# Kernel tuning notes

Measured on AMD Instinct MI355X. Metric: run time of the kernel, lower is better.

## Reference

```python
import jax, jax.numpy as jnp
import numpy as np

EPS = 1e-5  # BatchNorm1d eps


def _glorot(key, shape):
    fan_in, fan_out = shape[0], shape[1]
    lim = float(np.sqrt(6.0 / (fan_in + fan_out)))
    return jax.random.uniform(key, shape, jnp.float32, -lim, lim)


def setup_inputs() -> dict:
    key = jax.random.key(0)
    ks = jax.random.split(key, 6)
    N, IN, H, OUT = 50000, 128, 64, 64
    E = 800000
    x = jax.random.normal(ks[0], (N, IN), jnp.float32)
    edge_index = jax.random.randint(ks[1], (2, E), 0, N, jnp.int64)
    return {
        "x": x,
        "edge_index": edge_index,
        "W1": _glorot(ks[2], (IN, H)),
        "b1": jnp.zeros((H,), jnp.float32),
        "gamma1": jnp.ones((H,), jnp.float32),
        "beta1": jnp.zeros((H,), jnp.float32),
        "W2": _glorot(ks[3], (H, OUT)),
        "b2": jnp.zeros((OUT,), jnp.float32),
        "gamma2": jnp.ones((OUT,), jnp.float32),
        "beta2": jnp.zeros((OUT,), jnp.float32),
    }


def _gcn_conv(x, W, b, src, dst, norm, n):
    # x' = D^{-1/2} (A + I) D^{-1/2} X W + b  (PyG GCNConv, edge_weight=None)
    h = x @ W                              # [N, F]
    msg = h[src] * norm[:, None]           # gather + scale, [E+N, F]
    out = jax.ops.segment_sum(msg, dst, num_segments=n)  # scatter-add
    return out + b


def _batch_norm(h, gamma, beta):
    # training-mode BN over node dim, biased variance (as torch uses for normalization)
    mean = h.mean(0)
    var = h.var(0)
    return (h - mean) * jax.lax.rsqrt(var + EPS) * gamma + beta


def reference(x, edge_index, W1, b1, gamma1, beta1, W2, b2, gamma2, beta2):
    n = x.shape[0]
    # add self loops
    loop = jnp.arange(n, dtype=edge_index.dtype)
    src = jnp.concatenate([edge_index[0], loop])
    dst = jnp.concatenate([edge_index[1], loop])
    # symmetric degree normalization (deg >= 1 thanks to self loops)
    deg = jax.ops.segment_sum(jnp.ones(src.shape[0], x.dtype), dst, num_segments=n)
    dinv = jax.lax.rsqrt(jnp.maximum(deg, 1e-12))
    norm = dinv[src] * dinv[dst]           # [E+N]

    # layer 1: GCNConv -> BN -> ReLU (dropout = identity in eval)
    h = _gcn_conv(x, W1, b1, src, dst, norm, n)
    h = jax.nn.relu(_batch_norm(h, gamma1, beta1))
    # layer 2: GCNConv -> BN (no activation on last layer)
    h = _gcn_conv(h, W2, b2, src, dst, norm, n)
    h = _batch_norm(h, gamma2, beta2)
    return h
```

## Files before the change

### kernel.cpp

```cpp
#include <hip/hip_runtime.h>
#include <hip/hip_fp16.h>
#include <math.h>

#define EPS 1e-5f
#define CAP 64

typedef float v4f __attribute__((ext_vector_type(4)));

__device__ __forceinline__ float xor32sum(float a) {
    return a + __shfl_xor(a, 32, 64);
}

__global__ void k_init(int* __restrict__ cnt, float* __restrict__ stats,
                       __half* __restrict__ Ylo, __half* __restrict__ Yhi,
                       unsigned short* __restrict__ csr, int N) {
    int i = blockIdx.x * blockDim.x + threadIdx.x;
    if (i < N) {
        cnt[i] = 0;
        int4* p = (int4*)(csr + (size_t)i * CAP);
#pragma unroll
        for (int k = 0; k < 8; ++k) p[k] = make_int4(-1, -1, -1, -1);
    }
    if (i < 256) stats[i] = 0.0f;
    if (i < 16) {
        ((int*)(Ylo + (size_t)N * 32))[i] = 0;
        ((int*)(Yhi + (size_t)N * 32))[i] = 0;
    }
}

__global__ __launch_bounds__(256) void k_gemm1_fill(const float* __restrict__ x,
                                                    const float* __restrict__ W1,
                                                    __half* __restrict__ Ylo,
                                                    __half* __restrict__ Yhi, int N,
                                                    const int* __restrict__ src,
                                                    const int* __restrict__ dst,
                                                    int* __restrict__ cnt,
                                                    unsigned short* __restrict__ csr,
                                                    int E, int F, int G) {
    if ((int)blockIdx.x < F) {
        int t = blockIdx.x * 256 + threadIdx.x;
        int stride = F * 256;
        for (int e = t; e < E; e += stride) {
            int d = dst[e];
            int pos = atomicAdd(&cnt[d], 1);
            if (pos < CAP)
                __builtin_nontemporal_store((unsigned short)src[e], &csr[(size_t)d * CAP + pos]);
        }
        return;
    }
    __shared__ float w[128 * 64];
    __shared__ float xs[4][8][128];
    for (int i = threadIdx.x; i < 128 * 64; i += 256) w[i] = W1[i];
    __syncthreads();
    int lane = threadIdx.x & 63;
    int wave = threadIdx.x >> 6;
    int half = lane >> 5, l = lane & 31;
    __half* Yout = half ? Yhi : Ylo;
    int gwave = (blockIdx.x - F) * 4 + wave;
    int nw = G * 4;
    for (int r0 = gwave * 8; r0 < N; r0 += nw * 8) {
        int nr = min(8, N - r0);
        for (int j = 0; j < nr; ++j)
            *(float2*)&xs[wave][j][lane * 2] =
                *(const float2*)(x + (size_t)(r0 + j) * 128 + lane * 2);
        float acc[8];
#pragma unroll
        for (int j = 0; j < 8; ++j) acc[j] = 0.f;
#pragma unroll 4
        for (int kc = 0; kc < 32; ++kc) {
            const float* wp = &w[kc * 256 + lane];
            float wk0 = wp[0], wk1 = wp[64], wk2 = wp[128], wk3 = wp[192];
#pragma unroll
            for (int j = 0; j < 8; ++j) {
                float4 xv = *(const float4*)&xs[wave][j][kc * 4];
                acc[j] += xv.x * wk0 + xv.y * wk1 + xv.z * wk2 + xv.w * wk3;
            }
        }
#pragma unroll
        for (int j = 0; j < 8; ++j)
            if (j < nr) Yout[(size_t)(r0 + j) * 32 + l] = __float2half(acc[j]);
    }
}

__global__ void k_scale(const int* __restrict__ cnt, float* __restrict__ dinv,
                        __half* __restrict__ Ylo, __half* __restrict__ Yhi, int N) {
    int i = blockIdx.x * blockDim.x + threadIdx.x;
    if (i == 0) dinv[N] = 0.0f;
    int row = i >> 2, c4 = i & 3;
    if (row >= N) return;
    float dv = rsqrtf((float)(cnt[row] + 1));
    if (c4 == 0) dinv[row] = dv;
    union U16 { uint4 u; __half2 h[4]; } t;
#pragma unroll
    for (int buf = 0; buf < 2; ++buf) {
        __half* Y = buf ? Yhi : Ylo;
        uint4* p = (uint4*)(Y + (size_t)row * 32 + c4 * 8);
        t.u = *p;
#pragma unroll
        for (int k = 0; k < 4; ++k) {
            float2 f = __half22float2(t.h[k]);
            t.h[k] = __float22half2_rn(make_float2(f.x * dv, f.y * dv));
        }
        *p = t.u;
    }
}

__global__ __launch_bounds__(256) void k_agg(const __half* __restrict__ Ylo,
                                             const __half* __restrict__ Yhi,
                                             const unsigned short* __restrict__ csr,
                                             const int* __restrict__ cnt,
                                             const float* __restrict__ dinv,
                                             float* __restrict__ H,
                                             float* __restrict__ stats, int N) {
    __shared__ float ssum[4][32], ssq[4][32];
    int half = blockIdx.x & 1;
    const __half* Y = half ? Yhi : Ylo;
    int lane = threadIdx.x & 63;
    int wave = threadIdx.x >> 6;
    int fl = lane & 3;
    int node = (lane >> 2) & 3;
    int g = lane >> 4;
    int gd = g >> 1;
    int gsh = (g & 1) << 4;
    float selfmask = (g == 0) ? 1.f : 0.f;
    int slot = (blockIdx.x >> 1) * 4 + wave;
    int nslots = (gridDim.x >> 1) * 4;
    float s[8], q[8];
#pragma unroll
    for (int j = 0; j < 8; ++j) { s[j] = 0.f; q[j] = 0.f; }
    union U16 { uint4 u; __half2 h[4]; };
    for (int base = slot * 4; base < N; base += nslots * 4) {
        int myv = base + node;
        bool vok = myv < N;
        int vs = vok ? myv : N;
        int c  = vok ? min(cnt[myv], CAP) : 0;
        float dv = dinv[vs];
        const unsigned int* crow =
            (const unsigned int*)(csr + (size_t)(vok ? myv : 0) * CAP);
        float a[8];
        {
            U16 t; t.u = *(const uint4*)(Y + (size_t)vs * 32 + fl * 8);
#pragma unroll
            for (int k = 0; k < 4; ++k) {
                float2 f = __half22float2(t.h[k]);
                a[2 * k]     = selfmask * f.x;
                a[2 * k + 1] = selfmask * f.y;
            }
        }
        for (int b = 0; b < 16; ++b) {
            if (__all(4 * b >= c)) break;
            unsigned int w = crow[2 * b + gd];
            int ent = vok ? (int)((w >> gsh) & 0xFFFFu) : 0xFFFF;
            int idx = min(ent, N);
            U16 t; t.u = *(const uint4*)(Y + (size_t)idx * 32 + fl * 8);
#pragma unroll
            for (int k = 0; k < 4; ++k) {
                float2 f = __half22float2(t.h[k]);
                a[2 * k]     += f.x;
                a[2 * k + 1] += f.y;
            }
        }
#pragma unroll
        for (int j = 0; j < 8; ++j) {
            a[j] += __shfl_xor(a[j], 16, 64);
            a[j] = xor32sum(a[j]) * dv;
        }
        if (g == 0 && vok) {
            v4f lo = {a[0], a[1], a[2], a[3]};
            v4f hi = {a[4], a[5], a[6], a[7]};
            float* dst = H + (size_t)myv * 64 + half * 32 + fl * 8;
            __builtin_nontemporal_store(lo, (v4f*)dst);
            __builtin_nontemporal_store(hi, (v4f*)(dst + 4));
        }
#pragma unroll
        for (int j = 0; j < 8; ++j) { s[j] += a[j]; q[j] += a[j] * a[j]; }
    }
#pragma unroll
    for (int j = 0; j < 8; ++j) {
        s[j] += __shfl_xor(s[j], 4, 64); s[j] += __shfl_xor(s[j], 8, 64);
        q[j] += __shfl_xor(q[j], 4, 64); q[j] += __shfl_xor(q[j], 8, 64);
    }
    if (lane < 4) {
#pragma unroll
        for (int j = 0; j < 8; ++j) {
            ssum[wave][fl * 8 + j] = s[j];
            ssq[wave][fl * 8 + j]  = q[j];
        }
    }
    __syncthreads();
    if (threadIdx.x < 32) {
        float ts = ssum[0][threadIdx.x] + ssum[1][threadIdx.x] + ssum[2][threadIdx.x] + ssum[3][threadIdx.x];
        float tq = ssq[0][threadIdx.x] + ssq[1][threadIdx.x] + ssq[2][threadIdx.x] + ssq[3][threadIdx.x];
        atomicAdd(&stats[half * 32 + threadIdx.x], ts);
        atomicAdd(&stats[64 + half * 32 + threadIdx.x], tq);
    }
}

__global__ __launch_bounds__(256) void k_gemm2(const float* __restrict__ H1,
                                               const float* __restrict__ stats,
                                               const float* __restrict__ gamma,
                                               const float* __restrict__ beta,
                                               const float* __restrict__ W2,
                                               const float* __restrict__ dinv,
                                               __half* __restrict__ Ylo,
                                               __half* __restrict__ Yhi, int N) {
    __shared__ float w[64 * 64];
    __shared__ float xs[4][64][4];
    for (int i = threadIdx.x; i < 64 * 64; i += 256) w[i] = W2[i];
    int lane = threadIdx.x & 63;
    int wave = threadIdx.x >> 6;
    int half = lane >> 5, l = lane & 31;
    __half* Yout = half ? Yhi : Ylo;
    float mean = stats[lane] / (float)N;
    float var = stats[64 + lane] / (float)N - mean * mean;
    float rstd = rsqrtf(var + EPS);
    float scale = rstd * gamma[lane];
    float shift = beta[lane] - mean * scale;
    __syncthreads();
    int gwave = blockIdx.x * 4 + wave;
    int nw = gridDim.x * 4;
    for (int r0 = gwave * 4; r0 < N; r0 += nw * 4) {
        int nr = min(4, N - r0);
#pragma unroll
        for (int j = 0; j < 4; ++j) {
            float v = 0.f;
            if (j < nr) {
                v = H1[(size_t)(r0 + j) * 64 + lane];
                v = fmaxf(v * scale + shift, 0.f);
            }
            xs[wave][lane][j] = v;
        }
        float a0 = 0.f, a1 = 0.f, a2 = 0.f, a3 = 0.f;
#pragma unroll 8
        for (int k = 0; k < 64; ++k) {
            float wk = w[k * 64 + lane];
            float4 xv = *(const float4*)&xs[wave][k][0];
            a0 += xv.x * wk; a1 += xv.y * wk; a2 += xv.z * wk; a3 += xv.w * wk;
        }
        Yout[(size_t)(r0 + 0) * 32 + l] = __float2half(a0 * dinv[r0]);
        if (nr > 1) Yout[(size_t)(r0 + 1) * 32 + l] = __float2half(a1 * dinv[r0 + 1]);
        if (nr > 2) Yout[(size_t)(r0 + 2) * 32 + l] = __float2half(a2 * dinv[r0 + 2]);
        if (nr > 3) Yout[(size_t)(r0 + 3) * 32 + l] = __float2half(a3 * dinv[r0 + 3]);
    }
}

__global__ void k_bnfinal(float* __restrict__ out, const float* __restrict__ stats,
                          const float* __restrict__ gamma, const float* __restrict__ beta,
                          int N) {
    int i = blockIdx.x * blockDim.x + threadIdx.x;
    int total = N * 64;
    if (i < total) {
        int f = i & 63;
        float mean = stats[f] / (float)N;
        float var = stats[64 + f] / (float)N - mean * mean;
        float rstd = rsqrtf(var + EPS);
        out[i] = (out[i] - mean) * rstd * gamma[f] + beta[f];
    }
}

extern "C" void kernel_launch(void* const* d_in, const int* in_sizes, int n_in,
                              void* d_out, int out_size, void* d_ws, size_t ws_size,
                              hipStream_t stream) {
    const float* x      = (const float*)d_in[0];
    const int*   ei     = (const int*)d_in[1];
    const float* W1     = (const float*)d_in[2];
    const float* gamma1 = (const float*)d_in[4];
    const float* beta1  = (const float*)d_in[5];
    const float* W2     = (const float*)d_in[6];
    const float* gamma2 = (const float*)d_in[8];
    const float* beta2  = (const float*)d_in[9];
    float* out = (float*)d_out;

    const int N = in_sizes[0] / 128;
    const int E = in_sizes[1] / 2;
    const int* src = ei;
    const int* dst = ei + E;

    char* ws = (char*)d_ws;
    int*   cnt   = (int*)  ws;
    float* stats = (float*)(ws + 0x40000);
    float* dinv  = (float*)(ws + 0x50000);
    __half* Ylo  = (__half*)(ws + 0x90000);
    __half* Yhi  = (__half*)(ws + 0x90000 + 0x320000);
    float* H1    = (float*)(ws + 0x90000 + 0x640000);
    unsigned short* csr = (unsigned short*)(ws + 0x90000 + 0x640000 + 0xC40000);

    const int B = (N + 255) / 256;
    const int total = N * 64;
    const int G = 768, F = 256;

    k_init<<<B, 256, 0, stream>>>(cnt, stats, Ylo, Yhi, csr, N);

    k_gemm1_fill<<<F + G, 256, 0, stream>>>(x, W1, Ylo, Yhi, N, src, dst, cnt, csr, E, F, G);
    k_scale<<<(N * 4 + 255) / 256, 256, 0, stream>>>(cnt, dinv, Ylo, Yhi, N);
    k_agg<<<1250, 256, 0, stream>>>(Ylo, Yhi, csr, cnt, dinv, H1, stats, N);

    k_gemm2<<<1024, 256, 0, stream>>>(H1, stats, gamma1, beta1, W2, dinv, Ylo, Yhi, N);
    k_agg<<<1250, 256, 0, stream>>>(Ylo, Yhi, csr, cnt, dinv, out, stats + 128, N);
    k_bnfinal<<<(total + 255) / 256, 256, 0, stream>>>(out, stats + 128, gamma2, beta2, N);
}
```

Measured before the change: 267.3 us.

## Use MFMA f16 matrix cores for first-layer GEMM, rebalance fill blocks

Replaces the LDS-staged scalar FP32 X·W1 GEMM with MFMA 16x16x32 f16 instructions. W1 fragments are held in registers and x rows are converted to half on load. The number of blocks doing the CSR fill is also raised from 256 to 512. Inputs are now rounded to fp16 before the multiply, which may reduce accuracy, and the output store pattern becomes strided per lane.

Measured after the change: 259.1 us. 3.1% less time.

```diff
diff --git a/kernel.cpp b/kernel.cpp
--- a/kernel.cpp
+++ b/kernel.cpp
@@ -6,6 +6,8 @@
 #define CAP 64
 
 typedef float v4f __attribute__((ext_vector_type(4)));
+typedef _Float16 half8 __attribute__((ext_vector_type(8)));
+typedef float f32x4 __attribute__((ext_vector_type(4)));
 
 __device__ __forceinline__ float xor32sum(float a) {
     return a + __shfl_xor(a, 32, 64);
@@ -48,37 +50,54 @@
         }
         return;
     }
-    __shared__ float w[128 * 64];
-    __shared__ float xs[4][8][128];
-    for (int i = threadIdx.x; i < 128 * 64; i += 256) w[i] = W1[i];
-    __syncthreads();
     int lane = threadIdx.x & 63;
     int wave = threadIdx.x >> 6;
-    int half = lane >> 5, l = lane & 31;
-    __half* Yout = half ? Yhi : Ylo;
-    int gwave = (blockIdx.x - F) * 4 + wave;
-    int nw = G * 4;
-    for (int r0 = gwave * 8; r0 < N; r0 += nw * 8) {
-        int nr = min(8, N - r0);
-        for (int j = 0; j < nr; ++j)
-            *(float2*)&xs[wave][j][lane * 2] =
-                *(const float2*)(x + (size_t)(r0 + j) * 128 + lane * 2);
-        float acc[8];
-#pragma unroll
-        for (int j = 0; j < 8; ++j) acc[j] = 0.f;
-#pragma unroll 4
-        for (int kc = 0; kc < 32; ++kc) {
-            const float* wp = &w[kc * 256 + lane];
-            float wk0 = wp[0], wk1 = wp[64], wk2 = wp[128], wk3 = wp[192];
-#pragma unroll
-            for (int j = 0; j < 8; ++j) {
-                float4 xv = *(const float4*)&xs[wave][j][kc * 4];
-                acc[j] += xv.x * wk0 + xv.y * wk1 + xv.z * wk2 + xv.w * wk3;
+    int ln15 = lane & 15;
+    int kg = lane >> 4;
+    half8 Bf[4][4];
+#pragma unroll
+    for (int kt = 0; kt < 4; ++kt)
+#pragma unroll
+        for (int ct = 0; ct < 4; ++ct) {
+            half8 b;
+#pragma unroll
+            for (int j = 0; j < 8; ++j)
+                b[j] = (_Float16)W1[(size_t)(kt * 32 + kg * 8 + j) * 64 + ct * 16 + ln15];
+            Bf[kt][ct] = b;
+        }
+    int nrb = (N + 15) >> 4;
+    int gw = (blockIdx.x - F) * 4 + wave;
+    int nwv = G * 4;
+    for (int rb = gw; rb < nrb; rb += nwv) {
+        int row = min(rb * 16 + ln15, N - 1);
+        const float4* xr = (const float4*)(x + (size_t)row * 128);
+        f32x4 acc[4];
+#pragma unroll
+        for (int ct = 0; ct < 4; ++ct) acc[ct] = (f32x4){0.f, 0.f, 0.f, 0.f};
+#pragma unroll
+        for (int kt = 0; kt < 4; ++kt) {
+            float4 v0 = xr[kt * 8 + kg * 2];
+            float4 v1 = xr[kt * 8 + kg * 2 + 1];
+            half8 A;
+            A[0] = (_Float16)v0.x; A[1] = (_Float16)v0.y;
+            A[2] = (_Float16)v0.z; A[3] = (_Float16)v0.w;
+            A[4] = (_Float16)v1.x; A[5] = (_Float16)v1.y;
+            A[6] = (_Float16)v1.z; A[7] = (_Float16)v1.w;
+#pragma unroll
+            for (int ct = 0; ct < 4; ++ct)
+                acc[ct] = __builtin_amdgcn_mfma_f32_16x16x32_f16(A, Bf[kt][ct], acc[ct], 0, 0, 0);
+        }
+#pragma unroll
+        for (int ct = 0; ct < 4; ++ct) {
+            int col = ct * 16 + ln15;
+            __half* Yo = (col >= 32) ? Yhi : Ylo;
+            int cc = col & 31;
+#pragma unroll
+            for (int i = 0; i < 4; ++i) {
+                int gr = rb * 16 + kg * 4 + i;
+                if (gr < N) Yo[(size_t)gr * 32 + cc] = __float2half(acc[ct][i]);
             }
         }
-#pragma unroll
-        for (int j = 0; j < 8; ++j)
-            if (j < nr) Yout[(size_t)(r0 + j) * 32 + l] = __float2half(acc[j]);
     }
 }
 
@@ -287,7 +306,7 @@
 
     const int B = (N + 255) / 256;
     const int total = N * 64;
-    const int G = 768, F = 256;
+    const int G = 768, F = 512;
 
     k_init<<<B, 256, 0, stream>>>(cnt, stats, Ylo, Yhi, csr, N);
 
```
